# Optimization experiments

Hardware: AMD Instinct MI355X
Metric: run time of the kernel (lower is better)

## Reference

```python
import jax, jax.numpy as jnp
import numpy as np

N_WIN = 8  # matches init kwarg n_win

def setup_inputs() -> dict:
    key = jax.random.key(0)
    k1, k2, k3 = jax.random.split(key, 3)
    c = 64
    x = jax.random.normal(k1, (1, c, 256, 256), dtype=jnp.float32)
    W = jax.random.normal(k2, (3 * c, c), dtype=jnp.float32) * 0.05
    bias = jax.random.normal(k3, (3 * c,), dtype=jnp.float32) * 0.05
    return {"x": x, "W": W, "bias": bias}

def reference(x, W, bias):
    b, c, h, w = x.shape
    n_h = n_w = N_WIN
    hs, ws = h // n_h, w // n_w
    nw = n_h * n_w
    # unfold into non-overlapping windows: [1, nw, hs*ws, c]
    xw = x.reshape(b, c, n_h, hs, n_w, ws)
    xw = xw.transpose(0, 2, 4, 3, 5, 1).reshape(1, nw, hs * ws, c)
    # shared QKV linear
    qkv = xw @ W.T + bias
    q, k, v = qkv[..., :c], qkv[..., c:2 * c], qkv[..., 2 * c:3 * c]
    # region-level routing via mean-pooled tokens
    q_r = q.mean(axis=2)  # [1, nw, c]
    k_r = k.mean(axis=2)
    a_r = jax.nn.relu(jnp.einsum('bic,bjc->bij', q_r, k_r))  # [1, nw, nw]
    # mix windows: a_r @ flattened(k/q) == window-mixing einsum
    k_m = jnp.einsum('bij,bjtc->bitc', a_r, k)
    q_m = jnp.einsum('bij,bjtc->bitc', a_r, q)
    # relu-gated windowed attention
    attn = jax.nn.relu(jnp.einsum('bitc,bisc->bits', q_m, k_m))  # [1, nw, T, T]
    o = jnp.einsum('bits,bisc->bitc', attn, v)  # [1, nw, T, c]
    # fold back to image
    o = o.reshape(b, n_h, n_w, hs, ws, c).transpose(0, 5, 1, 3, 2, 4).reshape(b, c, h, w)
    return o
```

## Files before the change

kernel.cpp:

```cpp
#include <hip/hip_runtime.h>

typedef _Float16 half_t;
typedef __attribute__((ext_vector_type(8))) _Float16 half8;
typedef __attribute__((ext_vector_type(4))) _Float16 half4;
typedef __attribute__((ext_vector_type(4))) float floatx4;
typedef __attribute__((ext_vector_type(16))) float floatx16;

#define MFMA16(A, B, C) __builtin_amdgcn_mfma_f32_16x16x32_f16((A), (B), (C), 0, 0, 0)
#define MFMA32(A, B, C) __builtin_amdgcn_mfma_f32_32x32x16_f16((A), (B), (C), 0, 0, 0)

__global__ __launch_bounds__(256) void k_qkv(
    const float* __restrict__ x, const float* __restrict__ W,
    const float* __restrict__ bias, half_t* __restrict__ q,
    half_t* __restrict__ k, half_t* __restrict__ vT,
    float* __restrict__ qp, float* __restrict__ kp) {
  __shared__ __align__(16) half_t Xs[128][72];
  __shared__ __align__(16) half_t Ws[192][72];
  __shared__ float qs_l[64], ks_l[64];
  const int w = blockIdx.y;
  const int tx = blockIdx.x;
  const int t0 = tx * 128;
  const int ih = w >> 3, iw = w & 7;
  const int xbase = ih * 8192 + iw * 32;
  const int tid = threadIdx.x;

  for (int i = tid; i < 8192; i += 256) {
    const int c = i >> 7, tt = i & 127;
    const int t = t0 + tt;
    Xs[tt][c] = (half_t)x[c * 65536 + xbase + (t >> 5) * 256 + (t & 31)];
  }
  for (int i = tid; i < 3072; i += 256) {
    const int o = i >> 4, c4 = (i & 15) * 4;
    const floatx4 v = *(const floatx4*)&W[o * 64 + c4];
    half4 hv;
    #pragma unroll
    for (int p = 0; p < 4; p++) hv[p] = (half_t)v[p];
    *(half4*)&Ws[o][c4] = hv;
  }
  if (tid < 64) { qs_l[tid] = 0.f; ks_l[tid] = 0.f; }
  __syncthreads();

  const int wave = tid >> 6, lane = tid & 63;
  const int lrow = lane & 15, lq = lane >> 4;
  const int rbase = (wave >> 1) * 64;
  const int cbase = (wave & 1) * 96;

  floatx4 acc[4][6];
  const floatx4 z = {0.f, 0.f, 0.f, 0.f};
  #pragma unroll
  for (int mt = 0; mt < 4; mt++)
    #pragma unroll
    for (int nt = 0; nt < 6; nt++) acc[mt][nt] = z;

  #pragma unroll
  for (int kf = 0; kf < 2; kf++) {
    const int koff = kf * 32 + lq * 8;
    half8 a[4], b[6];
    #pragma unroll
    for (int mt = 0; mt < 4; mt++)
      a[mt] = *(const half8*)&Xs[rbase + mt * 16 + lrow][koff];
    #pragma unroll
    for (int nt = 0; nt < 6; nt++)
      b[nt] = *(const half8*)&Ws[cbase + nt * 16 + lrow][koff];
    #pragma unroll
    for (int mt = 0; mt < 4; mt++)
      #pragma unroll
      for (int nt = 0; nt < 6; nt++)
        acc[mt][nt] = MFMA16(a[mt], b[nt], acc[mt][nt]);
  }

  #pragma unroll
  for (int nt = 0; nt < 6; nt++) {
    const int o = cbase + nt * 16 + lrow;
    const float bs = bias[o];
    if (o < 64) {
      float s = 0.f;
      #pragma unroll
      for (int mt = 0; mt < 4; mt++) {
        const int tr = t0 + rbase + mt * 16 + lq * 4;
        #pragma unroll
        for (int r = 0; r < 4; r++) {
          const float v = acc[mt][nt][r] + bs;
          q[w * 65536 + (tr + r) * 64 + o] = (half_t)v;
          s += v;
        }
      }
      atomicAdd(&qs_l[o], s);
    } else if (o < 128) {
      const int oc = o - 64;
      float s = 0.f;
      #pragma unroll
      for (int mt = 0; mt < 4; mt++) {
        const int tr = t0 + rbase + mt * 16 + lq * 4;
        #pragma unroll
        for (int r = 0; r < 4; r++) {
          const float v = acc[mt][nt][r] + bs;
          k[w * 65536 + (tr + r) * 64 + oc] = (half_t)v;
          s += v;
        }
      }
      atomicAdd(&ks_l[oc], s);
    } else {
      const int oc = o - 128;
      #pragma unroll
      for (int mt = 0; mt < 4; mt++) {
        const int tr = t0 + rbase + mt * 16 + lq * 4;
        half4 pk;
        #pragma unroll
        for (int r = 0; r < 4; r++) pk[r] = (half_t)(acc[mt][nt][r] + bs);
        *(half4*)&vT[w * 65536 + oc * 1024 + tr] = pk;
      }
    }
  }
  __syncthreads();
  if (tid < 64) {
    qp[(w * 8 + tx) * 64 + tid] = qs_l[tid];
    kp[(w * 8 + tx) * 64 + tid] = ks_l[tid];
  }
}

__global__ __launch_bounds__(256) void k_ar(const float* __restrict__ qp,
                                            const float* __restrict__ kp,
                                            half_t* __restrict__ arH) {
  __shared__ float qs[64][65];
  __shared__ float ks[64][65];
  const int tid = threadIdx.x;
  for (int e = tid; e < 4096; e += 256) {
    const int i = e >> 6, c = e & 63;
    float sq = 0.f, sk = 0.f;
    #pragma unroll
    for (int t = 0; t < 8; t++) {
      sq += qp[i * 512 + t * 64 + c];
      sk += kp[i * 512 + t * 64 + c];
    }
    qs[i][c] = sq;
    ks[i][c] = sk;
  }
  __syncthreads();
  const float scale = 1.f / (1024.f * 1024.f);
  const int e = blockIdx.x * 256 + tid;
  const int i = e >> 6, j = e & 63;
  float s = 0.f;
  #pragma unroll
  for (int c = 0; c < 64; c++) s += qs[i][c] * ks[j][c];
  s *= scale;
  arH[e] = (half_t)(s > 0.f ? s : 0.f);
}

__global__ __launch_bounds__(256) void k_mix(const half_t* __restrict__ q,
                                             const half_t* __restrict__ k,
                                             const half_t* __restrict__ arH,
                                             half_t* __restrict__ qm,
                                             half_t* __restrict__ km) {
  const half_t* __restrict__ src = blockIdx.y ? k : q;
  half_t* __restrict__ dst = blockIdx.y ? km : qm;
  const int tid = threadIdx.x;
  const int wave = tid >> 6, lane = tid & 63;
  const int ln31 = lane & 31;
  const int hk8 = (lane >> 5) * 8;

  half8 aA[2][4];
  #pragma unroll
  for (int mt = 0; mt < 2; mt++)
    #pragma unroll
    for (int kk = 0; kk < 4; kk++)
      aA[mt][kk] = *(const half8*)&arH[(mt * 32 + ln31) * 64 + kk * 16 + hk8];

  #pragma unroll
  for (int t32 = 0; t32 < 2; t32++) {
    const int pos = blockIdx.x * 256 + wave * 64 + t32 * 32 + ln31;
    half8 bB[4];
    #pragma unroll
    for (int kk = 0; kk < 4; kk++)
      #pragma unroll
      for (int jj = 0; jj < 8; jj++)
        bB[kk][jj] = src[(kk * 16 + hk8 + jj) * 65536 + pos];

    floatx16 c0, c1;
    #pragma unroll
    for (int r = 0; r < 16; r++) { c0[r] = 0.f; c1[r] = 0.f; }
    #pragma unroll
    for (int kk = 0; kk < 4; kk++) {
      c0 = MFMA32(aA[0][kk], bB[kk], c0);
      c1 = MFMA32(aA[1][kk], bB[kk], c1);
    }
    const int h4 = (lane >> 5) * 4;
    #pragma unroll
    for (int r = 0; r < 16; r++) {
      const int row = (r & 3) + h4 + 8 * (r >> 2);
      dst[row * 65536 + pos] = (half_t)c0[r];
      dst[(32 + row) * 65536 + pos] = (half_t)c1[r];
    }
  }
}

__global__ __launch_bounds__(256, 2) void k_attn(const half_t* __restrict__ qm,
                                                 const half_t* __restrict__ km,
                                                 const half_t* __restrict__ vT,
                                                 float* __restrict__ out) {
  __shared__ __align__(16) half_t Vs[64][136];
  __shared__ __align__(16) half_t St[128][138];
  const int w = blockIdx.y;
  const int t0 = blockIdx.x * 128;
  const int tid = threadIdx.x;
  const int wave = tid >> 6, lane = tid & 63;
  const int ln31 = lane & 31;
  const int hk8 = (lane >> 5) * 8, hk4 = (lane >> 5) * 4;
  const int w32 = wave * 32;
  const int wbase = w * 65536;

  half8 bQ[4][4];
  #pragma unroll
  for (int tt = 0; tt < 4; tt++)
    #pragma unroll
    for (int kk = 0; kk < 4; kk++)
      bQ[tt][kk] = *(const half8*)&qm[wbase + (t0 + tt * 32 + ln31) * 64 + kk * 16 + hk8];

  floatx16 oacc[2];
  #pragma unroll
  for (int ct = 0; ct < 2; ct++)
    #pragma unroll
    for (int r = 0; r < 16; r++) oacc[ct][r] = 0.f;

  for (int sc = 0; sc < 8; sc++) {
    const int s0 = sc * 128;
    __syncthreads();
    for (int idx = tid; idx < 1024; idx += 256) {
      const int c = idx >> 4, so = (idx & 15) * 8;
      *(half8*)&Vs[c][so] = *(const half8*)&vT[wbase + c * 1024 + s0 + so];
    }
    half8 aK[4];
    #pragma unroll
    for (int kk = 0; kk < 4; kk++)
      aK[kk] = *(const half8*)&km[wbase + (s0 + w32 + ln31) * 64 + kk * 16 + hk8];
    __syncthreads();

    floatx16 sacc[4];
    #pragma unroll
    for (int tt = 0; tt < 4; tt++)
      #pragma unroll
      for (int r = 0; r < 16; r++) sacc[tt][r] = 0.f;
    #pragma unroll
    for (int kk = 0; kk < 4; kk++)
      #pragma unroll
      for (int tt = 0; tt < 4; tt++)
        sacc[tt] = MFMA32(aK[kk], bQ[tt][kk], sacc[tt]);

    #pragma unroll
    for (int tt = 0; tt < 4; tt++) {
      const int t = tt * 32 + ln31;
      #pragma unroll
      for (int g = 0; g < 4; g++) {
        const int s = w32 + g * 8 + hk4;
        half4 pk;
        #pragma unroll
        for (int p = 0; p < 4; p++) {
          const float v = sacc[tt][g * 4 + p];
          pk[p] = (half_t)(v > 0.f ? v : 0.f);
        }
        *(half4*)&St[t][s] = pk;
      }
    }
    __syncthreads();

    #pragma unroll
    for (int kk = 0; kk < 8; kk++) {
      const half8 bS = *(const half8*)&St[w32 + ln31][kk * 16 + hk8];
      #pragma unroll
      for (int ct = 0; ct < 2; ct++) {
        const half8 aV = *(const half8*)&Vs[ct * 32 + ln31][kk * 16 + hk8];
        oacc[ct] = MFMA32(aV, bS, oacc[ct]);
      }
    }
  }

  const int ih = w >> 3, iw = w & 7;
  const int obase = ih * 8192 + iw * 32;
  const int tb = ((t0 + w32) >> 5) * 256 + ln31;
  const int h4 = (lane >> 5) * 4;
  #pragma unroll
  for (int ct = 0; ct < 2; ct++) {
    #pragma unroll
    for (int r = 0; r < 16; r++) {
      const int c = ct * 32 + (r & 3) + h4 + 8 * (r >> 2);
      out[c * 65536 + obase + tb] = oacc[ct][r];
    }
  }
}

extern "C" void kernel_launch(void* const* d_in, const int* in_sizes, int n_in,
                              void* d_out, int out_size, void* d_ws, size_t ws_size,
                              hipStream_t stream) {
  const float* x = (const float*)d_in[0];
  const float* W = (const float*)d_in[1];
  const float* bias = (const float*)d_in[2];
  float* out = (float*)d_out;

  half_t* q = (half_t*)d_ws;
  half_t* k = q + 4194304;
  half_t* vT = k + 4194304;
  half_t* qm = vT + 4194304;
  half_t* km = qm + 4194304;
  float* qp = (float*)(km + 4194304);
  float* kp = qp + 32768;
  half_t* arH = (half_t*)(kp + 32768);

  k_qkv<<<dim3(8, 64), 256, 0, stream>>>(x, W, bias, q, k, vT, qp, kp);
  k_ar<<<16, 256, 0, stream>>>(qp, kp, arH);
  k_mix<<<dim3(256, 2), 256, 0, stream>>>(q, k, arH, qm, km);
  k_attn<<<dim3(8, 64), 256, 0, stream>>>(qm, km, vT, out);
}
```

Baseline: 128.7 us.

## Stage QKV outputs through LDS, fold routing matrix into mix kernel, reorder attn grid

The QKV kernel now writes q/k/vT tiles into shared memory first and then stores them to global memory with coalesced 16-byte vectors, replacing scattered 2-byte and 8-byte stores. The separate routing-matrix kernel is removed. Each mix block now recomputes the 64x64 relu routing matrix from the partial sums with MFMA in LDS, and issues its first global loads before that work to hide the latency. The attention grid swaps x/y so blocks from different windows run together. This removes one launch and improves store coalescing, at the cost of every mix block redundantly recomputing the routing matrix and reducing the partial sums.

```diff
diff --git a/kernel.cpp b/kernel.cpp
--- a/kernel.cpp
+++ b/kernel.cpp
@@ -14,9 +14,13 @@
     const float* __restrict__ bias, half_t* __restrict__ q,
     half_t* __restrict__ k, half_t* __restrict__ vT,
     float* __restrict__ qp, float* __restrict__ kp) {
-  __shared__ __align__(16) half_t Xs[128][72];
-  __shared__ __align__(16) half_t Ws[192][72];
-  __shared__ float qs_l[64], ks_l[64];
+  __shared__ __align__(16) char smem[52736];
+  half_t(*Xs)[72] = (half_t(*)[72])smem;
+  half_t(*Ws)[72] = (half_t(*)[72])(smem + 18432);
+  half_t(*S1)[136] = (half_t(*)[136])smem;
+  half_t(*S2)[136] = (half_t(*)[136])(smem + 34816);
+  float* qs_l = (float*)(smem + 52224);
+  float* ks_l = qs_l + 64;
   const int w = blockIdx.y;
   const int tx = blockIdx.x;
   const int t0 = tx * 128;
@@ -68,113 +72,149 @@
       for (int nt = 0; nt < 6; nt++)
         acc[mt][nt] = MFMA16(a[mt], b[nt], acc[mt][nt]);
   }
+  __syncthreads();
 
   #pragma unroll
   for (int nt = 0; nt < 6; nt++) {
     const int o = cbase + nt * 16 + lrow;
     const float bs = bias[o];
-    if (o < 64) {
+    if (o < 128) {
       float s = 0.f;
       #pragma unroll
       for (int mt = 0; mt < 4; mt++) {
-        const int tr = t0 + rbase + mt * 16 + lq * 4;
+        const int tr = rbase + mt * 16 + lq * 4;
         #pragma unroll
         for (int r = 0; r < 4; r++) {
           const float v = acc[mt][nt][r] + bs;
-          q[w * 65536 + (tr + r) * 64 + o] = (half_t)v;
+          S1[tr + r][o] = (half_t)v;
           s += v;
         }
       }
-      atomicAdd(&qs_l[o], s);
-    } else if (o < 128) {
-      const int oc = o - 64;
-      float s = 0.f;
-      #pragma unroll
-      for (int mt = 0; mt < 4; mt++) {
-        const int tr = t0 + rbase + mt * 16 + lq * 4;
-        #pragma unroll
-        for (int r = 0; r < 4; r++) {
-          const float v = acc[mt][nt][r] + bs;
-          k[w * 65536 + (tr + r) * 64 + oc] = (half_t)v;
-          s += v;
-        }
-      }
-      atomicAdd(&ks_l[oc], s);
+      if (o < 64) atomicAdd(&qs_l[o], s);
+      else atomicAdd(&ks_l[o - 64], s);
     } else {
       const int oc = o - 128;
       #pragma unroll
       for (int mt = 0; mt < 4; mt++) {
-        const int tr = t0 + rbase + mt * 16 + lq * 4;
+        const int tr = rbase + mt * 16 + lq * 4;
         half4 pk;
         #pragma unroll
         for (int r = 0; r < 4; r++) pk[r] = (half_t)(acc[mt][nt][r] + bs);
-        *(half4*)&vT[w * 65536 + oc * 1024 + tr] = pk;
-      }
-    }
-  }
-  __syncthreads();
+        *(half4*)&S2[oc][tr] = pk;
+      }
+    }
+  }
+  __syncthreads();
+
+  for (int idx = tid; idx < 3072; idx += 256) {
+    if (idx < 2048) {
+      const int t = idx >> 4, seg = idx & 15;
+      const half8 v = *(const half8*)&S1[t][seg * 8];
+      if (seg < 8)
+        *(half8*)&q[w * 65536 + (t0 + t) * 64 + seg * 8] = v;
+      else
+        *(half8*)&k[w * 65536 + (t0 + t) * 64 + (seg - 8) * 8] = v;
+    } else {
+      const int i2 = idx - 2048;
+      const int oc = i2 >> 4, seg = i2 & 15;
+      *(half8*)&vT[w * 65536 + oc * 1024 + t0 + seg * 8] =
+          *(const half8*)&S2[oc][seg * 8];
+    }
+  }
   if (tid < 64) {
     qp[(w * 8 + tx) * 64 + tid] = qs_l[tid];
     kp[(w * 8 + tx) * 64 + tid] = ks_l[tid];
   }
 }
 
-__global__ __launch_bounds__(256) void k_ar(const float* __restrict__ qp,
-                                            const float* __restrict__ kp,
-                                            half_t* __restrict__ arH) {
-  __shared__ float qs[64][65];
-  __shared__ float ks[64][65];
-  const int tid = threadIdx.x;
-  for (int e = tid; e < 4096; e += 256) {
-    const int i = e >> 6, c = e & 63;
-    float sq = 0.f, sk = 0.f;
-    #pragma unroll
-    for (int t = 0; t < 8; t++) {
-      sq += qp[i * 512 + t * 64 + c];
-      sk += kp[i * 512 + t * 64 + c];
-    }
-    qs[i][c] = sq;
-    ks[i][c] = sk;
-  }
-  __syncthreads();
-  const float scale = 1.f / (1024.f * 1024.f);
-  const int e = blockIdx.x * 256 + tid;
-  const int i = e >> 6, j = e & 63;
-  float s = 0.f;
-  #pragma unroll
-  for (int c = 0; c < 64; c++) s += qs[i][c] * ks[j][c];
-  s *= scale;
-  arH[e] = (half_t)(s > 0.f ? s : 0.f);
-}
-
 __global__ __launch_bounds__(256) void k_mix(const half_t* __restrict__ q,
                                              const half_t* __restrict__ k,
-                                             const half_t* __restrict__ arH,
+                                             const float* __restrict__ qp,
+                                             const float* __restrict__ kp,
                                              half_t* __restrict__ qm,
                                              half_t* __restrict__ km) {
+  __shared__ __align__(16) half_t qh[64][72];
+  __shared__ __align__(16) half_t kh[64][72];
+  __shared__ __align__(16) half_t arL[64][72];
   const half_t* __restrict__ src = blockIdx.y ? k : q;
   half_t* __restrict__ dst = blockIdx.y ? km : qm;
   const int tid = threadIdx.x;
   const int wave = tid >> 6, lane = tid & 63;
   const int ln31 = lane & 31;
   const int hk8 = (lane >> 5) * 8;
+  const int lrow = lane & 15, lq = lane >> 4;
+
+  const int pos0 = blockIdx.x * 256 + wave * 64 + ln31;
+  half8 bB0[4];
+  #pragma unroll
+  for (int kk = 0; kk < 4; kk++)
+    #pragma unroll
+    for (int jj = 0; jj < 8; jj++)
+      bB0[kk][jj] = src[(kk * 16 + hk8 + jj) * 65536 + pos0];
+
+  for (int e = tid; e < 1024; e += 256) {
+    const int i = e >> 4, c4 = (e & 15) * 4;
+    floatx4 sq = {0.f, 0.f, 0.f, 0.f}, sk = {0.f, 0.f, 0.f, 0.f};
+    #pragma unroll
+    for (int t = 0; t < 8; t++) {
+      sq += *(const floatx4*)&qp[i * 512 + t * 64 + c4];
+      sk += *(const floatx4*)&kp[i * 512 + t * 64 + c4];
+    }
+    #pragma unroll
+    for (int p = 0; p < 4; p++) {
+      qh[i][c4 + p] = (half_t)sq[p];
+      kh[i][c4 + p] = (half_t)sk[p];
+    }
+  }
+  __syncthreads();
+
+  {
+    floatx4 ac[4];
+    const floatx4 z = {0.f, 0.f, 0.f, 0.f};
+    #pragma unroll
+    for (int nt = 0; nt < 4; nt++) ac[nt] = z;
+    #pragma unroll
+    for (int kf = 0; kf < 2; kf++) {
+      const int koff = kf * 32 + lq * 8;
+      const half8 aF = *(const half8*)&qh[wave * 16 + lrow][koff];
+      #pragma unroll
+      for (int nt = 0; nt < 4; nt++) {
+        const half8 bF = *(const half8*)&kh[nt * 16 + lrow][koff];
+        ac[nt] = MFMA16(aF, bF, ac[nt]);
+      }
+    }
+    const float scale = 1.f / (1024.f * 1024.f);
+    #pragma unroll
+    for (int nt = 0; nt < 4; nt++)
+      #pragma unroll
+      for (int r = 0; r < 4; r++) {
+        const float v = ac[nt][r] * scale;
+        arL[wave * 16 + lq * 4 + r][nt * 16 + lrow] = (half_t)(v > 0.f ? v : 0.f);
+      }
+  }
+  __syncthreads();
 
   half8 aA[2][4];
   #pragma unroll
   for (int mt = 0; mt < 2; mt++)
     #pragma unroll
     for (int kk = 0; kk < 4; kk++)
-      aA[mt][kk] = *(const half8*)&arH[(mt * 32 + ln31) * 64 + kk * 16 + hk8];
+      aA[mt][kk] = *(const half8*)&arL[mt * 32 + ln31][kk * 16 + hk8];
 
   #pragma unroll
   for (int t32 = 0; t32 < 2; t32++) {
     const int pos = blockIdx.x * 256 + wave * 64 + t32 * 32 + ln31;
     half8 bB[4];
-    #pragma unroll
-    for (int kk = 0; kk < 4; kk++)
-      #pragma unroll
-      for (int jj = 0; jj < 8; jj++)
-        bB[kk][jj] = src[(kk * 16 + hk8 + jj) * 65536 + pos];
+    if (t32 == 0) {
+      #pragma unroll
+      for (int kk = 0; kk < 4; kk++) bB[kk] = bB0[kk];
+    } else {
+      #pragma unroll
+      for (int kk = 0; kk < 4; kk++)
+        #pragma unroll
+        for (int jj = 0; jj < 8; jj++)
+          bB[kk][jj] = src[(kk * 16 + hk8 + jj) * 65536 + pos];
+    }
 
     floatx16 c0, c1;
     #pragma unroll
@@ -200,8 +240,8 @@
                                                  float* __restrict__ out) {
   __shared__ __align__(16) half_t Vs[64][136];
   __shared__ __align__(16) half_t St[128][138];
-  const int w = blockIdx.y;
-  const int t0 = blockIdx.x * 128;
+  const int w = blockIdx.x;
+  const int t0 = blockIdx.y * 128;
   const int tid = threadIdx.x;
   const int wave = tid >> 6, lane = tid & 63;
   const int ln31 = lane & 31;
@@ -303,10 +343,8 @@
   half_t* km = qm + 4194304;
   float* qp = (float*)(km + 4194304);
   float* kp = qp + 32768;
-  half_t* arH = (half_t*)(kp + 32768);
 
   k_qkv<<<dim3(8, 64), 256, 0, stream>>>(x, W, bias, q, k, vT, qp, kp);
-  k_ar<<<16, 256, 0, stream>>>(qp, kp, arH);
-  k_mix<<<dim3(256, 2), 256, 0, stream>>>(q, k, arH, qm, km);
-  k_attn<<<dim3(8, 64), 256, 0, stream>>>(qm, km, vT, out);
+  k_mix<<<dim3(256, 2), 256, 0, stream>>>(q, k, qp, kp, qm, km);
+  k_attn<<<dim3(64, 8), 256, 0, stream>>>(qm, km, vT, out);
 }
```

Result: faster. 124.0 us (-3.6%).
